# Kernel optimization log

Measured on AMD Instinct MI355X. Metric: run time of the kernel, lower is better.

## Reference

```python
import jax, jax.numpy as jnp
import numpy as np
import math

BINS = 32  # quantization_bins


def setup_inputs() -> dict:
    key = jax.random.key(0)
    k1, k2 = jax.random.split(key)
    coords = jax.random.normal(k1, (4, 1024, 2), dtype=jnp.float32)
    # TruncatedNormal(stddev=0.02) init for the learnable table; plain normal*0.02 is fine for a numeric reference
    rpe_table = jax.random.normal(k2, (2 * BINS, 16), dtype=jnp.float32) * 0.02
    return {"coords": coords, "rpe_table": rpe_table}


def reference(coords, rpe_table):
    bins = BINS
    half = bins // 2
    eta = coords[..., 0]  # [B,T]
    phi = coords[..., 1]  # [B,T]
    rel_eta = eta[:, :, None] - eta[:, None, :]  # [B,T,T]
    rel_phi = phi[:, :, None] - phi[:, None, :]  # [B,T,T]
    pi = jnp.asarray(math.pi, dtype=phi.dtype)
    # wrap phi difference to (-pi, pi]; jnp.mod matches tf.math.floormod for floats
    rel_phi = jnp.mod(rel_phi + pi, 2 * pi) - pi
    eta_range = jnp.maximum(jnp.max(jnp.abs(rel_eta)), jnp.asarray(1e-06, eta.dtype))
    phi_range = pi
    # tf.cast float->int32 truncates toward zero, same as astype(int32)
    eta_bins = (rel_eta / eta_range * half).astype(jnp.int32)
    phi_bins = (rel_phi / phi_range * half).astype(jnp.int32)
    eta_bins = jnp.clip(eta_bins, -half, half - 1)
    phi_bins = jnp.clip(phi_bins, -half, half - 1)
    eta_idx = eta_bins + half               # [B,T,T] in [0, bins)
    phi_idx = phi_bins + half + bins        # [B,T,T] in [bins, 2*bins)
    eta_bias = rpe_table[eta_idx]           # [B,T,T,H]
    phi_bias = rpe_table[phi_idx]           # [B,T,T,H]
    bias = eta_bias + phi_bias
    return jnp.transpose(bias, (0, 3, 1, 2))  # [B,H,T,T]
```

## Files before the change

kernel.cpp:

```cpp
#include <hip/hip_runtime.h>
#include <math.h>

#define BB 4
#define TT 1024
#define HH 16
#define NROWS 64

#define PI_F    3.14159265358979323846f
#define TWOPI_F 6.28318530717958647692f

__global__ void QuantizedRPE_range_kernel(const float* __restrict__ coords,
                                          float* __restrict__ ws) {
    int lane = threadIdx.x & 63;
    int b = threadIdx.x >> 6;
    float mx = -1e30f, mn = 1e30f;
    for (int t = lane; t < TT; t += 64) {
        float e = coords[(size_t)(b * TT + t) * 2];
        mx = fmaxf(mx, e);
        mn = fminf(mn, e);
    }
    #pragma unroll
    for (int m = 32; m; m >>= 1) {
        mx = fmaxf(mx, __shfl_xor(mx, m));
        mn = fminf(mn, __shfl_xor(mn, m));
    }
    __shared__ float sr[BB];
    if (lane == 0) sr[b] = mx - mn;
    __syncthreads();
    if (threadIdx.x == 0) {
        float r = fmaxf(fmaxf(sr[0], sr[1]), fmaxf(sr[2], sr[3]));
        ws[0] = fmaxf(r, 1e-6f);
    }
}

__global__ __launch_bounds__(256) void QuantizedRPE_fill_kernel(
        const float* __restrict__ coords,
        const float* __restrict__ table,
        const float* __restrict__ ws,
        float* __restrict__ out) {
    __shared__ float tl[HH][65];
    int tid = threadIdx.x;
    #pragma unroll
    for (int k = tid; k < NROWS * HH; k += 256) {
        int idx = k >> 4, h = k & 15;
        tl[h][idx] = table[k];
    }

    float range = ws[0];
    int b = blockIdx.x >> 10;
    int i = blockIdx.x & (TT - 1);
    float ei  = coords[(size_t)(b * TT + i) * 2 + 0];
    float pii = coords[(size_t)(b * TT + i) * 2 + 1];
    __syncthreads();

    int j0 = tid * 4;
    const float4* cp = (const float4*)(coords + (size_t)(b * TT + j0) * 2);
    float4 c01 = cp[0];
    float4 c23 = cp[1];
    float ej[4] = {c01.x, c01.z, c23.x, c23.z};
    float pj[4] = {c01.y, c01.w, c23.y, c23.w};

    int eidx[4], pidx[4];
    #pragma unroll
    for (int jj = 0; jj < 4; ++jj) {
        float re = ei - ej[jj];
        int be = (int)(re / range * 16.0f);
        be = min(max(be, -16), 15);
        eidx[jj] = be + 16;
        float w = (pii - pj[jj]) + PI_F;
        float m = fmodf(w, TWOPI_F);
        if (m < 0.0f) m += TWOPI_F;
        float rp = m - PI_F;
        int bp = (int)(rp / PI_F * 16.0f);
        bp = min(max(bp, -16), 15);
        pidx[jj] = bp + 48;
    }

    float* op = out + ((size_t)(b * HH) * TT + i) * TT + j0;
    #pragma unroll
    for (int q = 0; q < 4; ++q) {
        #pragma unroll
        for (int r = 0; r < 4; ++r) {
            int h = q * 4 + r;
            float4 v;
            v.x = tl[h][eidx[0]] + tl[h][pidx[0]];
            v.y = tl[h][eidx[1]] + tl[h][pidx[1]];
            v.z = tl[h][eidx[2]] + tl[h][pidx[2]];
            v.w = tl[h][eidx[3]] + tl[h][pidx[3]];
            *(float4*)(op + (size_t)h * TT * TT) = v;
        }
    }
}

extern "C" void kernel_launch(void* const* d_in, const int* in_sizes, int n_in,
                              void* d_out, int out_size, void* d_ws, size_t ws_size,
                              hipStream_t stream) {
    const float* coords = (const float*)d_in[0];
    const float* table  = (const float*)d_in[1];
    float* out = (float*)d_out;
    float* ws  = (float*)d_ws;

    QuantizedRPE_range_kernel<<<1, 256, 0, stream>>>(coords, ws);
    QuantizedRPE_fill_kernel<<<BB * TT, 256, 0, stream>>>(coords, table, ws, out);
}
```

Before: 55.39 us.

## Fuse range reduction into fill kernel and use nontemporal vector stores

Removes the separate single-block range kernel by having every fill block recompute the global eta range from all coords, so the output kernel needs no second launch and no workspace dependency. The table is stored row-major with padding, so each pair of bins is read as vectorized LDS loads, and outputs are written with nontemporal stores. The trade-off is redundant per-block reads of 16 KB of coords (cached) and a reduction in each of the 4096 blocks.

```diff
diff --git a/kernel.cpp b/kernel.cpp
--- a/kernel.cpp
+++ b/kernel.cpp
@@ -5,90 +5,93 @@
 #define TT 1024
 #define HH 16
 #define NROWS 64
+#define RPAD 20
 
 #define PI_F    3.14159265358979323846f
 #define TWOPI_F 6.28318530717958647692f
 
-__global__ void QuantizedRPE_range_kernel(const float* __restrict__ coords,
-                                          float* __restrict__ ws) {
-    int lane = threadIdx.x & 63;
-    int b = threadIdx.x >> 6;
-    float mx = -1e30f, mn = 1e30f;
-    for (int t = lane; t < TT; t += 64) {
-        float e = coords[(size_t)(b * TT + t) * 2];
-        mx = fmaxf(mx, e);
-        mn = fminf(mn, e);
-    }
-    #pragma unroll
-    for (int m = 32; m; m >>= 1) {
-        mx = fmaxf(mx, __shfl_xor(mx, m));
-        mn = fminf(mn, __shfl_xor(mn, m));
-    }
-    __shared__ float sr[BB];
-    if (lane == 0) sr[b] = mx - mn;
-    __syncthreads();
-    if (threadIdx.x == 0) {
-        float r = fmaxf(fmaxf(sr[0], sr[1]), fmaxf(sr[2], sr[3]));
-        ws[0] = fmaxf(r, 1e-6f);
-    }
-}
+typedef float f4 __attribute__((ext_vector_type(4)));
 
-__global__ __launch_bounds__(256) void QuantizedRPE_fill_kernel(
+__global__ __launch_bounds__(256, 4) void QuantizedRPE_fused_kernel(
         const float* __restrict__ coords,
         const float* __restrict__ table,
-        const float* __restrict__ ws,
         float* __restrict__ out) {
-    __shared__ float tl[HH][65];
+    __shared__ float tl[NROWS][RPAD];
+    __shared__ float sre[BB];
     int tid = threadIdx.x;
-    #pragma unroll
-    for (int k = tid; k < NROWS * HH; k += 256) {
-        int idx = k >> 4, h = k & 15;
-        tl[h][idx] = table[k];
+
+    {
+        f4 t4 = ((const f4*)table)[tid];
+        int row = tid >> 2, col = (tid & 3) * 4;
+        *(f4*)&tl[row][col] = t4;
     }
 
-    float range = ws[0];
+    {
+        int lane = tid & 63;
+        int w = tid >> 6;
+        float mx = -1e30f, mn = 1e30f;
+        #pragma unroll
+        for (int it = 0; it < TT / 64; ++it) {
+            int t = lane + it * 64;
+            float e = coords[(size_t)(w * TT + t) * 2];
+            mx = fmaxf(mx, e);
+            mn = fminf(mn, e);
+        }
+        #pragma unroll
+        for (int m = 32; m; m >>= 1) {
+            mx = fmaxf(mx, __shfl_xor(mx, m));
+            mn = fminf(mn, __shfl_xor(mn, m));
+        }
+        if (lane == 0) sre[w] = mx - mn;
+    }
+    __syncthreads();
+    float range = fmaxf(fmaxf(fmaxf(sre[0], sre[1]), fmaxf(sre[2], sre[3])), 1e-6f);
+
     int b = blockIdx.x >> 10;
     int i = blockIdx.x & (TT - 1);
     float ei  = coords[(size_t)(b * TT + i) * 2 + 0];
     float pii = coords[(size_t)(b * TT + i) * 2 + 1];
-    __syncthreads();
 
     int j0 = tid * 4;
-    const float4* cp = (const float4*)(coords + (size_t)(b * TT + j0) * 2);
-    float4 c01 = cp[0];
-    float4 c23 = cp[1];
+    const f4* cp = (const f4*)(coords + (size_t)(b * TT + j0) * 2);
+    f4 c01 = cp[0];
+    f4 c23 = cp[1];
     float ej[4] = {c01.x, c01.z, c23.x, c23.z};
     float pj[4] = {c01.y, c01.w, c23.y, c23.w};
 
-    int eidx[4], pidx[4];
+    float s[4][16];
     #pragma unroll
     for (int jj = 0; jj < 4; ++jj) {
         float re = ei - ej[jj];
         int be = (int)(re / range * 16.0f);
         be = min(max(be, -16), 15);
-        eidx[jj] = be + 16;
+        int eidx = be + 16;
         float w = (pii - pj[jj]) + PI_F;
         float m = fmodf(w, TWOPI_F);
         if (m < 0.0f) m += TWOPI_F;
         float rp = m - PI_F;
         int bp = (int)(rp / PI_F * 16.0f);
         bp = min(max(bp, -16), 15);
-        pidx[jj] = bp + 48;
+        int pidx = bp + 48;
+
+        const f4* er = (const f4*)&tl[eidx][0];
+        const f4* pr = (const f4*)&tl[pidx][0];
+        #pragma unroll
+        for (int q = 0; q < 4; ++q) {
+            f4 a = er[q];
+            f4 c = pr[q];
+            s[jj][q * 4 + 0] = a.x + c.x;
+            s[jj][q * 4 + 1] = a.y + c.y;
+            s[jj][q * 4 + 2] = a.z + c.z;
+            s[jj][q * 4 + 3] = a.w + c.w;
+        }
     }
 
     float* op = out + ((size_t)(b * HH) * TT + i) * TT + j0;
     #pragma unroll
-    for (int q = 0; q < 4; ++q) {
-        #pragma unroll
-        for (int r = 0; r < 4; ++r) {
-            int h = q * 4 + r;
-            float4 v;
-            v.x = tl[h][eidx[0]] + tl[h][pidx[0]];
-            v.y = tl[h][eidx[1]] + tl[h][pidx[1]];
-            v.z = tl[h][eidx[2]] + tl[h][pidx[2]];
-            v.w = tl[h][eidx[3]] + tl[h][pidx[3]];
-            *(float4*)(op + (size_t)h * TT * TT) = v;
-        }
+    for (int h = 0; h < HH; ++h) {
+        f4 v = {s[0][h], s[1][h], s[2][h], s[3][h]};
+        __builtin_nontemporal_store(v, (f4*)(op + (size_t)h * TT * TT));
     }
 }
 
@@ -98,8 +101,7 @@
     const float* coords = (const float*)d_in[0];
     const float* table  = (const float*)d_in[1];
     float* out = (float*)d_out;
-    float* ws  = (float*)d_ws;
+    (void)d_ws; (void)ws_size;
 
-    QuantizedRPE_range_kernel<<<1, 256, 0, stream>>>(coords, ws);
-    QuantizedRPE_fill_kernel<<<BB * TT, 256, 0, stream>>>(coords, table, ws, out);
+    QuantizedRPE_fused_kernel<<<BB * TT, 256, 0, stream>>>(coords, table, out);
 }
```

New measurement: 65.91 us. +19.0%, slower.
